# Kernel optimization log

Hardware: AMD Instinct MI355X
Metric: run time of the kernel (lower is better)

Reference implementation:

```python
import jax, jax.numpy as jnp
import numpy as np

NAMES = ['tempo', 'chord', 'barbeat', 'type', 'pitch', 'duration', 'velocity']
VOCABS = [56, 135, 18, 4, 87, 18, 25]
EMBS = [128, 256, 64, 32, 512, 128, 128]
B, S, D, H, L, FF = 2, 2048, 512, 8, 8, 2048
HD = D // H
EPS = 1e-6


def _layernorm(x, g, b):
    m = x.mean(-1, keepdims=True)
    v = ((x - m) ** 2).mean(-1, keepdims=True)
    return (x - m) / jnp.sqrt(v + 1e-5) * g + b


def _rope(x, cos, sin):
    x1, x2 = jnp.split(x, 2, -1)
    return x * cos + jnp.concatenate([-x2, x1], -1) * sin


def _causal_linear_attn(q, k, v):
    # kernelized causal linear attention: phi = elu + 1, cumulative-sum normalization
    q = jax.nn.elu(q) + 1.0
    k = jax.nn.elu(k) + 1.0
    kv = jnp.cumsum(jnp.einsum('bshd,bshm->bshdm', k, v), axis=1)  # [B,S,H,HD,HD]
    z = 1.0 / (jnp.einsum('bshd,bshd->bsh', q, jnp.cumsum(k, axis=1)) + EPS)
    return jnp.einsum('bshd,bshdm->bshm', q, kv) * z[..., None]


def _forward(inputs, target, emb_tables, in_W, in_b, Wq, bq, Wk, bk, Wv, bv, Wo, bo,
             ln1_g, ln1_b, ln2_g, ln2_b, W1, b1, W2, b2, norm_g, norm_b, pWs, pbs, catW, catb):
    # multi-field embedding, each scaled by sqrt(d_emb) (CPEmbedding)
    embs = [emb_tables[i][inputs[..., i]] * jnp.sqrt(jnp.float32(EMBS[i])) for i in range(7)]
    x = jnp.concatenate(embs, -1) @ in_W + in_b  # [B,S,D]
    # PositionalEncoding: original indexes pe at position seq_len -> single d_model vector
    div = jnp.exp(jnp.arange(0, D, 2, dtype=jnp.float32) * (-np.log(10000.0) / D))
    pe = jnp.zeros((D,), jnp.float32).at[0::2].set(jnp.sin(S * div)).at[1::2].set(jnp.cos(S * div))
    x = x + pe
    # rotary tables for head_dim
    inv_freq = 1.0 / (10000.0 ** (jnp.arange(0, HD, 2, dtype=jnp.float32) / HD))
    fr = jnp.arange(S, dtype=jnp.float32)[:, None] * inv_freq[None, :]
    ang = jnp.concatenate([fr, fr], -1)  # [S,HD]
    cos = jnp.cos(ang)[None, :, None, :]
    sin = jnp.sin(ang)[None, :, None, :]
    for l in range(L):
        q = (x @ Wq[l] + bq[l]).reshape(B, S, H, HD)
        k = (x @ Wk[l] + bk[l]).reshape(B, S, H, HD)
        v = (x @ Wv[l] + bv[l]).reshape(B, S, H, HD)
        q = _rope(q, cos, sin)
        k = _rope(k, cos, sin)
        a = _causal_linear_attn(q, k, v).reshape(B, S, D) @ Wo[l] + bo[l]
        x = x + a
        y = x = _layernorm(x, ln1_g[l], ln1_b[l])
        y = jax.nn.gelu(y @ W1[l] + b1[l], approximate=False) @ W2[l] + b2[l]
        x = _layernorm(x + y, ln2_g[l], ln2_b[l])
    x = _layernorm(x, norm_g, norm_b)
    # MultiProj with teacher-forced type embedding (target branch)
    emb_t = emb_tables[3][target[..., 3]] * jnp.sqrt(jnp.float32(EMBS[3]))
    proj_type = (x @ pWs[3] + pbs[3]) * jnp.sqrt(jnp.float32(VOCABS[3]))  # from pre-concat x
    xc = jnp.concatenate([x, emb_t], -1) @ catW + catb
    outs = []
    for i in range(7):
        if i == 3:
            outs.append(proj_type)
        else:
            outs.append((xc @ pWs[i] + pbs[i]) * jnp.sqrt(jnp.float32(VOCABS[i])))
    return jnp.concatenate(outs, -1)  # [B,S,sum(VOCABS)=343]


def setup_inputs():
    key = jax.random.key(0)
    kit = iter(jax.random.split(key, 64))
    s = 0.02
    d = {}
    d['inputs'] = jax.random.randint(next(kit), (B, S, 7), 0, 4)
    d['target'] = jax.random.randint(next(kit), (B, S, 7), 0, 4)
    for i, n in enumerate(NAMES):
        d['emb_' + n] = jax.random.normal(next(kit), (VOCABS[i], EMBS[i]), jnp.float32) * s
    E = sum(EMBS)
    d['in_W'] = jax.random.normal(next(kit), (E, D)) * s
    d['in_b'] = jnp.zeros((D,))
    for nm, sh in [('Wq', (L, D, D)), ('Wk', (L, D, D)), ('Wv', (L, D, D)), ('Wo', (L, D, D)), ('W1', (L, D, FF)), ('W2', (L, FF, D))]:
        d[nm] = jax.random.normal(next(kit), sh) * s
    for nm, sh in [('bq', (L, D)), ('bk', (L, D)), ('bv', (L, D)), ('bo', (L, D)), ('b1', (L, FF)), ('b2', (L, D)), ('ln1_b', (L, D)), ('ln2_b', (L, D)), ('norm_b', (D,)), ('catb', (D,))]:
        d[nm] = jnp.zeros(sh)
    d['ln1_g'] = jnp.ones((L, D))
    d['ln2_g'] = jnp.ones((L, D))
    d['norm_g'] = jnp.ones((D,))
    for i, n in enumerate(NAMES):
        d['pW_' + n] = jax.random.normal(next(kit), (D, VOCABS[i])) * s
        d['pb_' + n] = jnp.zeros((VOCABS[i],))
    d['catW'] = jax.random.normal(next(kit), (D + 32, D)) * s
    return d


def reference(inputs, target, emb_tempo, emb_chord, emb_barbeat, emb_type, emb_pitch, emb_duration, emb_velocity,
              in_W, in_b, Wq, bq, Wk, bk, Wv, bv, Wo, bo, ln1_g, ln1_b, ln2_g, ln2_b, W1, b1, W2, b2,
              norm_g, norm_b, pW_tempo, pb_tempo, pW_chord, pb_chord, pW_barbeat, pb_barbeat, pW_type, pb_type,
              pW_pitch, pb_pitch, pW_duration, pb_duration, pW_velocity, pb_velocity, catW, catb):
    emb_tables = [emb_tempo, emb_chord, emb_barbeat, emb_type, emb_pitch, emb_duration, emb_velocity]
    pWs = [pW_tempo, pW_chord, pW_barbeat, pW_type, pW_pitch, pW_duration, pW_velocity]
    pbs = [pb_tempo, pb_chord, pb_barbeat, pb_type, pb_pitch, pb_duration, pb_velocity]
    return _forward(inputs, target, emb_tables, in_W, in_b, Wq, bq, Wk, bk, Wv, bv, Wo, bo,
                    ln1_g, ln1_b, ln2_g, ln2_b, W1, b1, W2, b2, norm_g, norm_b, pWs, pbs, catW, catb)
```

## Files before the change

kernel.cpp:

```cpp
#include <hip/hip_runtime.h>
#include <math.h>

typedef unsigned short u16;
typedef short bf16x8 __attribute__((ext_vector_type(8)));
typedef float f32x4 __attribute__((ext_vector_type(4)));
typedef u16 u16x4 __attribute__((ext_vector_type(4)));
typedef u16 u16x8 __attribute__((ext_vector_type(8)));

#define NB 2
#define NS 2048
#define ND 512
#define NH 8
#define NHD 64
#define NL 8
#define NFF 2048
#define NM (NB*NS)
#define NE 1248
#define NEP 1280
#define NXC 576
#define CHK 64
#define NCH (NS/CHK)
#define QKVW 1536

__device__ inline float b2f(u16 u){ union{ unsigned int i; float f;} x; x.i = ((unsigned int)u)<<16; return x.f; }
__device__ inline u16 f2b(float f){ union{ float f; unsigned int i;} x; x.f=f; unsigned int r = x.i + 0x7fffu + ((x.i>>16)&1u); return (u16)(r>>16); }

#define GLL(src, dst) __builtin_amdgcn_global_load_lds( \
    (__attribute__((address_space(1))) void*)(void*)(src), \
    (__attribute__((address_space(3))) void*)(dst), 16, 0, 0)

__global__ void k_embed(const int* __restrict__ inp,
    const float* __restrict__ e0, const float* __restrict__ e1, const float* __restrict__ e2,
    const float* __restrict__ e3, const float* __restrict__ e4, const float* __restrict__ e5,
    const float* __restrict__ e6, u16* __restrict__ xe)
{
  int row = blockIdx.x;
  int i0 = inp[row*7+0], i1 = inp[row*7+1], i2 = inp[row*7+2], i3 = inp[row*7+3],
      i4 = inp[row*7+4], i5 = inp[row*7+5], i6 = inp[row*7+6];
  size_t base = (size_t)row*NEP;
  for (int c = threadIdx.x; c < NEP; c += 256){
    float val = 0.f;
    if      (c < 128)  val = e0[i0*128 + c]        * 11.3137084990f;
    else if (c < 384)  val = e1[i1*256 + (c-128)]  * 16.0f;
    else if (c < 448)  val = e2[i2*64  + (c-384)]  * 8.0f;
    else if (c < 480)  val = e3[i3*32  + (c-448)]  * 5.6568542495f;
    else if (c < 992)  val = e4[i4*512 + (c-480)]  * 22.6274169980f;
    else if (c < 1120) val = e5[i5*128 + (c-992)]  * 11.3137084990f;
    else if (c < NE)   val = e6[i6*128 + (c-1120)] * 11.3137084990f;
    xe[base + c] = f2b(val);
  }
}

__device__ inline void trans_tile128(const float* __restrict__ W, u16* __restrict__ WT,
                                     int K, int N, int Kpad, int bx, int by){
  __shared__ u16 t[128*128];
  int tid = threadIdx.x;
  int k0 = by*128, n0 = bx*128;
  int c = tid & 31, sub = tid >> 5;
  #pragma unroll
  for (int half=0; half<2; half++){
    int kg = sub + half*8;
    u16 r0[8], r1[8], r2[8], r3[8];
    #pragma unroll
    for (int j=0;j<8;j++){
      int k = k0 + kg*8 + j;
      float4 v = {0.f,0.f,0.f,0.f};
      if (k < K) v = *(const float4*)(W + (size_t)k*N + n0 + c*4);
      r0[j] = f2b(v.x); r1[j] = f2b(v.y); r2[j] = f2b(v.z); r3[j] = f2b(v.w);
    }
    #pragma unroll
    for (int i=0;i<4;i++){
      int n = c*4 + i;
      int g = kg ^ (n & 15);
      const u16* rp = (i==0)?r0:(i==1)?r1:(i==2)?r2:r3;
      *(u16x8*)&t[n*128 + g*8] = *(const u16x8*)rp;
    }
  }
  __syncthreads();
  int kg2 = tid & 15, nsub = tid >> 4;
  #pragma unroll
  for (int p=0;p<8;p++){
    int nl = p*16 + nsub;
    int k = k0 + kg2*8;
    if (k < Kpad)
      *(u16x8*)(WT + (size_t)(n0+nl)*Kpad + k) = *(const u16x8*)&t[nl*128 + ((kg2 ^ (nl&15))<<3)];
  }
}

__global__ void k_prepw(const float* __restrict__ Wq, const float* __restrict__ Wk,
                        const float* __restrict__ Wv, const float* __restrict__ Wo,
                        const float* __restrict__ in_W, const float* __restrict__ catW,
                        const float* __restrict__ W1, const float* __restrict__ W2,
                        u16* __restrict__ qkvoT, u16* __restrict__ inWT, u16* __restrict__ catWT,
                        u16* __restrict__ w1T, u16* __restrict__ w2T)
{
  int bid = blockIdx.x;
  if (bid < 512){
    int z = bid >> 4, r = bid & 15;
    int l = z >> 2, s2 = z & 3;
    const float* W = (s2==0?Wq:s2==1?Wk:s2==2?Wv:Wo) + (size_t)l*ND*ND;
    trans_tile128(W, qkvoT + (size_t)z*ND*ND, ND, ND, ND, r & 3, r >> 2);
  } else if (bid < 552){
    int r = bid - 512;
    trans_tile128(in_W, inWT, NE, ND, NEP, r & 3, r >> 2);
  } else if (bid < 572){
    int r = bid - 552;
    trans_tile128(catW, catWT, 544, ND, NXC, r & 3, r >> 2);
  } else if (bid < 1084){
    int r = bid - 572;
    int l = r >> 6; int rr = r & 63;
    trans_tile128(W1 + (size_t)l*ND*NFF, w1T + (size_t)l*ND*NFF, ND, NFF, ND, rr & 15, rr >> 4);
  } else {
    int r = bid - 1084;
    int l = r >> 6; int rr = r & 63;
    trans_tile128(W2 + (size_t)l*NFF*ND, w2T + (size_t)l*ND*NFF, NFF, ND, NFF, rr & 3, rr >> 2);
  }
}

__global__ void k_misc(float* __restrict__ rc, float* __restrict__ rs,
    const float* p0,const float* p1,const float* p2,const float* p3,
    const float* p4,const float* p5,const float* p6,
    const float* q0,const float* q1,const float* q2,const float* q3,
    const float* q4,const float* q5,const float* q6,
    u16* __restrict__ pwcT, float* __restrict__ pbc,
    u16* __restrict__ ptT, float* __restrict__ pbt,
    const float* __restrict__ bq, const float* __restrict__ bk, const float* __restrict__ bv,
    float* __restrict__ bqkv, const float* __restrict__ in_b, float* __restrict__ bias_in)
{
  int idx = blockIdx.x*256 + threadIdx.x;
  if (idx < NS*32){
    int s = idx >> 5, j = idx & 31;
    double inv = exp(-(double)(2*j) * log(10000.0) / (double)NHD);
    double ang = (double)s * inv;
    rc[idx] = (float)cos(ang);
    rs[idx] = (float)sin(ang);
  }
  const int off[8] = {0,56,191,209,213,300,318,343};
  {
    int col = idx >> 9, k = idx & 511;
    if (col < 384){
      u16 v = 0;
      if (col < 343){
        int f = 0;
        while (col >= off[f+1]) f++;
        int cc = col - off[f];
        int V = off[f+1]-off[f];
        const float* P = (f==0)?p0:(f==1)?p1:(f==2)?p2:(f==3)?p3:(f==4)?p4:(f==5)?p5:p6;
        v = f2b(P[(size_t)k*V + cc] * sqrtf((float)V));
      }
      pwcT[(size_t)col*512 + k] = v;
    }
    if (idx < 64*512){
      int n = idx >> 9;
      ptT[idx] = (n < 4) ? f2b(p3[(size_t)k*4 + n]*2.0f) : (u16)0;
    }
  }
  if (idx < 343){
    int c2 = idx, f = 0;
    while (c2 >= off[f+1]) f++;
    int cc = c2 - off[f]; int V = off[f+1]-off[f];
    const float* Q = (f==0)?q0:(f==1)?q1:(f==2)?q2:(f==3)?q3:(f==4)?q4:(f==5)?q5:q6;
    pbc[idx] = Q[cc]*sqrtf((float)V);
  }
  if (idx < 4) pbt[idx] = q3[idx]*2.0f;
  if (idx < NL*QKVW){
    int l = idx / QKVW, c = idx % QKVW;
    float v = (c < 512) ? bq[l*512 + c] : (c < 1024) ? bk[l*512 + c - 512] : bv[l*512 + c - 1024];
    bqkv[idx] = v;
  }
  if (idx < ND){
    double div = exp(-(double)(idx & ~1) * log(10000.0) / (double)ND);
    double ang = (double)NS * div;
    float pev = (idx & 1) ? (float)cos(ang) : (float)sin(ang);
    bias_in[idx] = in_b[idx] + pev;
  }
}

template<int ACT, int NT, int TM>
__global__ __launch_bounds__(256) void k_gemm(
    const u16* __restrict__ A, const u16* __restrict__ BT,
    const float* __restrict__ bias, float* __restrict__ Cf, u16* __restrict__ Cb,
    int N, int klen, int lda, int ldb, int ldc,
    int koff, float* __restrict__ Cf2,
    const float* __restrict__ rc, const float* __restrict__ rs)
{
  constexpr int MREP = TM/32;
  __shared__ u16 SH[TM*64 + NT*32*64];
  u16* As = SH;
  u16* Bs = SH + TM*64;
  int tid = threadIdx.x;
  int w = tid >> 6, lane = tid & 63;

  int kz = blockIdx.z;
  A  += (size_t)kz*koff;
  BT += (size_t)kz*koff;
  if (kz){ Cf = Cf2; bias = nullptr; }

  int nwg = gridDim.x*gridDim.y;
  int d = blockIdx.y*gridDim.x + blockIdx.x;
  int wl = ((nwg & 7) == 0) ? ((d & 7)*(nwg >> 3) + (d >> 3)) : d;
  int bx = wl % gridDim.x, by = wl / gridDim.x;
  int m0 = by*TM, n0 = bx*(NT*32);

  f32x4 acc[MREP][NT];
  #pragma unroll
  for (int m=0;m<MREP;m++)
    #pragma unroll
    for (int n=0;n<NT;n++) acc[m][n] = (f32x4){0.f,0.f,0.f,0.f};

  int lg = lane>>3;
  int cg = (lane&7) ^ lg;
  const u16* ag = A  + (size_t)(m0 + w*(TM/4) + lg)*lda + cg*8;
  const u16* bg = BT + (size_t)(n0 + w*(NT*8) + lg)*ldb + cg*8;
  int wr = (w>>1)*(TM/2), wc = (w&1)*(NT*16);
  int lr = lane & 15;
  int rx = lr & 7;
  int cb_ = lane >> 4;
  int g = lane >> 4;

  int nk = klen >> 6;
  for (int t = 0; t < nk; ++t){
    int k0 = t << 6;
    #pragma unroll
    for (int i=0;i<TM/32;i++)
      GLL(ag + (size_t)(i*8)*lda + k0, &As[(w*(TM/4) + i*8)*64]);
    #pragma unroll
    for (int j=0;j<NT;j++)
      GLL(bg + (size_t)(j*8)*ldb + k0, &Bs[(w*(NT*8) + j*8)*64]);
    __syncthreads();
    #pragma unroll
    for (int kk=0;kk<2;kk++){
      int gA = ((kk*4 + cb_) ^ rx) * 8;
      bf16x8 af[MREP], bfr[NT];
      #pragma unroll
      for (int m=0;m<MREP;m++) af[m]  = *(const bf16x8*)&As[(wr + m*16 + lr)*64 + gA];
      #pragma unroll
      for (int n=0;n<NT;n++)   bfr[n] = *(const bf16x8*)&Bs[(wc + n*16 + lr)*64 + gA];
      #pragma unroll
      for (int m=0;m<MREP;m++)
        #pragma unroll
        for (int n=0;n<NT;n++)
          acc[m][n] = __builtin_amdgcn_mfma_f32_16x16x32_bf16(af[m], bfr[n], acc[m][n], 0,0,0);
    }
    __syncthreads();
  }

  if (ACT == 2){
    float* Cs = (float*)SH;
    #pragma unroll
    for (int n=0;n<NT;n++){
      int col = wc + n*16 + lr;
      float bv = bias ? bias[n0 + col] : 0.f;
      #pragma unroll
      for (int m=0;m<MREP;m++)
        #pragma unroll
        for (int r=0;r<4;r++)
          Cs[(wr + m*16 + g*4 + r)*64 + col] = acc[m][n][r] + bv;
    }
    __syncthreads();
    if (n0 < 1024){
      #pragma unroll
      for (int i=0;i<8;i++){
        int p = tid + i*256;
        int row = p >> 5, j = p & 31;
        float a1 = Cs[row*64 + j], a2 = Cs[row*64 + j + 32];
        int s = (m0 + row) & (NS-1);
        float c = rc[s*32+j], sn = rs[s*32+j];
        float r1 = a1*c - a2*sn, r2 = a2*c + a1*sn;
        Cb[(size_t)(m0+row)*ldc + n0 + j]      = f2b((r1 > 0.f) ? r1+1.f : expf(r1));
        Cb[(size_t)(m0+row)*ldc + n0 + j + 32] = f2b((r2 > 0.f) ? r2+1.f : expf(r2));
      }
    } else {
      #pragma unroll
      for (int i=0;i<16;i++){
        int p = tid + i*256;
        int row = p >> 6, c2 = p & 63;
        Cb[(size_t)(m0+row)*ldc + n0 + c2] = f2b(Cs[row*64 + c2]);
      }
    }
    return;
  }

  #pragma unroll
  for (int n=0;n<NT;n++){
    int col = n0 + wc + n*16 + lr;
    if (col < N){
      float bv = bias ? bias[col] : 0.f;
      #pragma unroll
      for (int m=0;m<MREP;m++){
        #pragma unroll
        for (int r=0;r<4;r++){
          int row = m0 + wr + m*16 + g*4 + r;
          float v = acc[m][n][r] + bv;
          if (ACT==1) v = 0.5f*v*(1.f+erff(v*0.70710678118654752f));
          if (Cf) Cf[(size_t)row*ldc + col] = v;
          if (Cb) Cb[(size_t)row*ldc + col] = f2b(v);
        }
      }
    }
  }
}

__global__ __launch_bounds__(256) void k_att1(const u16* __restrict__ qkv, float* __restrict__ pref){
  int c = blockIdx.x, h = blockIdx.y, b = blockIdx.z;
  __shared__ u16 Kt[64*64];
  __shared__ u16 Vt[80*64];
  int tid = threadIdx.x;
  {
    int t = tid & 63, dseg = (tid>>6)*16;
    const u16* kg = qkv + ((size_t)(b*NS + c*CHK + t))*QKVW + 512 + h*NHD + dseg;
    u16x8 k0 = *(const u16x8*)kg;
    u16x8 k1 = *(const u16x8*)(kg+8);
    u16x8 v0 = *(const u16x8*)(kg+512);
    u16x8 v1 = *(const u16x8*)(kg+520);
    #pragma unroll
    for (int e=0;e<8;e++){
      int d0 = dseg+e, d1 = dseg+8+e;
      Kt[(d0*64+t) ^ ((d0&7)<<3)] = k0[e];
      Kt[(d1*64+t) ^ ((d1&7)<<3)] = k1[e];
      Vt[(d0*64+t) ^ ((d0&7)<<3)] = v0[e];
      Vt[(d1*64+t) ^ ((d1&7)<<3)] = v1[e];
    }
    if (tid < 64) Vt[4096 + tid] = 0x3F80;
    for (int e = tid; e < 15*64; e += 256){
      int r = 65 + (e>>6), tt = e&63;
      Vt[(r*64+tt) ^ ((r&7)<<3)] = 0;
    }
  }
  __syncthreads();
  int lane = tid & 63, w = tid >> 6;
  int lr = lane & 15, lk = (lane>>4)*8;
  f32x4 acc[5];
  #pragma unroll
  for (int i=0;i<5;i++) acc[i] = (f32x4){0.f,0.f,0.f,0.f};
  #pragma unroll
  for (int kk=0;kk<2;kk++){
    int mcol = w*16 + lr;
    bf16x8 bfrag = *(const bf16x8*)&Kt[(mcol*64 + kk*32 + lk) ^ ((mcol&7)<<3)];
    #pragma unroll
    for (int fr=0; fr<5; fr++){
      int arow = fr*16 + lr;
      bf16x8 afrag = *(const bf16x8*)&Vt[(arow*64 + kk*32 + lk) ^ ((arow&7)<<3)];
      acc[fr] = __builtin_amdgcn_mfma_f32_16x16x32_bf16(afrag, bfrag, acc[fr], 0,0,0);
    }
  }
  size_t base = (((size_t)(b*NH + h))*NCH + c)*5120;
  int g = lane>>4;
  #pragma unroll
  for (int fr=0; fr<5; fr++)
    #pragma unroll
    for (int r=0;r<4;r++)
      pref[base + (fr*16 + g*4 + r)*64 + w*16 + lr] = acc[fr][r];
}

__global__ __launch_bounds__(256) void k_att2(const float* __restrict__ pref, u16* __restrict__ prefb){
  int bh = blockIdx.y;
  int e = blockIdx.x*256 + threadIdx.x;
  size_t base = (size_t)bh*NCH*5120 + e;
  int se = e ^ (((e>>6)&7)<<3);
  size_t sb = (size_t)bh*NCH*5120 + se;
  float v[NCH];
  #pragma unroll
  for (int c=0;c<NCH;c++) v[c] = pref[base + (size_t)c*5120];
  float run = 0.f;
  #pragma unroll
  for (int c=0;c<NCH;c++){ prefb[sb + (size_t)c*5120] = f2b(run); run += v[c]; }
}

__global__ __launch_bounds__(256) void k_att3(const u16* __restrict__ qkv,
    const u16* __restrict__ prefb, u16* __restrict__ outa)
{
  int c = blockIdx.x, h = blockIdx.y, b = blockIdx.z;
  __shared__ u16 Qs[4096], Ks[4096];
  __shared__ u16 Vt[5120], Ps[5120];
  __shared__ float dens[64];
  u16* Sm = Ks;
  int tid = threadIdx.x;
  int lane = tid & 63, w = tid >> 6;
  {
    int r8 = lane >> 3;
    int gsw = (lane & 7) ^ r8;
    const u16* qbase = qkv + ((size_t)(b*NS + c*CHK))*QKVW + h*NHD + gsw*8;
    #pragma unroll
    for (int half = 0; half < 2; half++){
      int rbase = w*16 + half*8;
      const u16* src = qbase + (size_t)(rbase + r8)*QKVW;
      GLL(src,       &Qs[rbase*64]);
      GLL(src + 512, &Ks[rbase*64]);
    }
    const u16* pb = prefb + (((size_t)(b*NH + h))*NCH + c)*5120 + lane*8;
    for (int ch = w; ch < 10; ch += 4)
      GLL(pb + ch*512, &Ps[ch*512]);
  }
  {
    int t = tid&63, dseg = (tid>>6)*16;
    const u16* vg = qkv + ((size_t)(b*NS + c*CHK + t))*QKVW + 1024 + h*NHD + dseg;
    u16x8 v0 = *(const u16x8*)vg;
    u16x8 v1 = *(const u16x8*)(vg+8);
    #pragma unroll
    for (int e=0;e<8;e++){
      int d0=dseg+e, d1=dseg+8+e;
      Vt[(d0*64+t)^((d0&7)<<3)] = v0[e];
      Vt[(d1*64+t)^((d1&7)<<3)] = v1[e];
    }
    if (tid<64) Vt[4096+tid] = 0x3F80;
    for (int e=tid; e<15*64; e+=256){
      int r = 65+(e>>6), tt = e&63;
      Vt[(r*64+tt)^((r&7)<<3)] = 0;
    }
  }
  __syncthreads();
  int lr = lane&15, lk = (lane>>4)*8, g = lane>>4;
  f32x4 sacc[4];
  #pragma unroll
  for (int i=0;i<4;i++) sacc[i] = (f32x4){0.f,0.f,0.f,0.f};
  int iq = w*16 + lr;
  #pragma unroll
  for (int kk=0;kk<2;kk++){
    bf16x8 bq = *(const bf16x8*)&Qs[(iq*64 + kk*32 + lk) ^ ((iq&7)<<3)];
    #pragma unroll
    for (int ft=0; ft<4; ft++){
      int tr = ft*16 + lr;
      bf16x8 ak = *(const bf16x8*)&Ks[(tr*64 + kk*32 + lk) ^ ((tr&7)<<3)];
      sacc[ft] = __builtin_amdgcn_mfma_f32_16x16x32_bf16(ak, bq, sacc[ft], 0,0,0);
    }
  }
  __syncthreads();
  #pragma unroll
  for (int ft=0; ft<4; ft++){
    int t0 = ft*16 + g*4;
    u16x4 pk;
    #pragma unroll
    for (int r=0;r<4;r++) pk[r] = f2b((t0+r <= iq) ? sacc[ft][r] : 0.f);
    *(u16x4*)&Sm[(iq*64 + t0) ^ ((iq&7)<<3)] = pk;
  }
  __syncthreads();
  f32x4 acc[5];
  #pragma unroll
  for (int i=0;i<5;i++) acc[i] = (f32x4){0.f,0.f,0.f,0.f};
  #pragma unroll
  for (int kk=0;kk<2;kk++){
    int sw = (iq&7)<<3;
    bf16x8 as = *(const bf16x8*)&Sm[(iq*64 + kk*32 + lk) ^ sw];
    bf16x8 aq = *(const bf16x8*)&Qs[(iq*64 + kk*32 + lk) ^ sw];
    #pragma unroll
    for (int c5=0;c5<5;c5++){
      int col = c5*16 + lr, sw2 = (col&7)<<3;
      bf16x8 bv = *(const bf16x8*)&Vt[(col*64 + kk*32 + lk) ^ sw2];
      bf16x8 bp = *(const bf16x8*)&Ps[(col*64 + kk*32 + lk) ^ sw2];
      acc[c5] = __builtin_amdgcn_mfma_f32_16x16x32_bf16(as, bv, acc[c5], 0,0,0);
      acc[c5] = __builtin_amdgcn_mfma_f32_16x16x32_bf16(aq, bp, acc[c5], 0,0,0);
    }
  }
  if (lr == 0){
    #pragma unroll
    for (int r=0;r<4;r++) dens[w*16 + g*4 + r] = acc[4][r];
  }
  __syncthreads();
  #pragma unroll
  for (int c5=0;c5<4;c5++){
    #pragma unroll
    for (int r=0;r<4;r++){
      int i = w*16 + g*4 + r;
      float z = 1.f/(dens[i] + 1e-6f);
      outa[((size_t)(b*NS + c*CHK + i))*ND + h*NHD + c5*16 + lr] = f2b(acc[c5][r]*z);
    }
  }
}

__global__ __launch_bounds__(256) void k_ln(const float* __restrict__ xin, const float* __restrict__ res,
    const float* __restrict__ res2, float* __restrict__ outx, u16* __restrict__ outb,
    const float* __restrict__ g, const float* __restrict__ bvec,
    const int* __restrict__ tgt, const float* __restrict__ embt, u16* __restrict__ xcb)
{
  int row = blockIdx.x, tid = threadIdx.x;
  size_t base = (size_t)row*ND;
  float v0 = xin[base+tid], v1 = xin[base+tid+256];
  if (res){ v0 += res[base+tid]; v1 += res[base+tid+256]; }
  if (res2){ v0 += res2[base+tid]; v1 += res2[base+tid+256]; }
  float s = v0+v1, ss2 = v0*v0 + v1*v1;
  #pragma unroll
  for (int o = 32; o >= 1; o >>= 1){
    s   += __shfl_down(s, o, 64);
    ss2 += __shfl_down(ss2, o, 64);
  }
  __shared__ float red[8];
  int wv = tid >> 6, ln = tid & 63;
  if (ln == 0){ red[wv] = s; red[4+wv] = ss2; }
  __syncthreads();
  float stot  = red[0]+red[1]+red[2]+red[3];
  float sstot = red[4]+red[5]+red[6]+red[7];
  float mean = stot * (1.0f/ND);
  float var  = sstot * (1.0f/ND) - mean*mean;
  float inv = 1.0f / sqrtf(var + 1e-5f);
  float o0 = (v0-mean)*inv*g[tid]     + bvec[tid];
  float o1 = (v1-mean)*inv*g[tid+256] + bvec[tid+256];
  outx[base+tid] = o0; outx[base+tid+256] = o1;
  if (outb){ outb[base+tid] = f2b(o0); outb[base+tid+256] = f2b(o1); }
  if (xcb){
    size_t xbse = (size_t)row*NXC;
    xcb[xbse+tid] = f2b(o0);
    xcb[xbse+tid+256] = f2b(o1);
    if (tid < 32){
      int id = tgt[row*7+3];
      xcb[xbse+512+tid] = f2b(embt[id*32+tid]*5.6568542495f);
      xcb[xbse+544+tid] = 0;
    }
  }
}

extern "C" void kernel_launch(void* const* d_in, const int* in_sizes, int n_in,
                              void* d_out, int out_size, void* d_ws, size_t ws_size,
                              hipStream_t stream)
{
  const int* inputs = (const int*)d_in[0];
  const int* target = (const int*)d_in[1];
  const float* emb[7];
  for (int i=0;i<7;i++) emb[i] = (const float*)d_in[2+i];
  const float* in_W  = (const float*)d_in[9];
  const float* in_b  = (const float*)d_in[10];
  const float* Wq = (const float*)d_in[11];
  const float* Wk = (const float*)d_in[12];
  const float* Wv = (const float*)d_in[13];
  const float* Wo = (const float*)d_in[14];
  const float* W1 = (const float*)d_in[15];
  const float* W2 = (const float*)d_in[16];
  const float* bq = (const float*)d_in[17];
  const float* bk = (const float*)d_in[18];
  const float* bv = (const float*)d_in[19];
  const float* bo = (const float*)d_in[20];
  const float* b1 = (const float*)d_in[21];
  const float* b2 = (const float*)d_in[22];
  const float* ln1_b = (const float*)d_in[23];
  const float* ln2_b = (const float*)d_in[24];
  const float* norm_b = (const float*)d_in[25];
  const float* catb   = (const float*)d_in[26];
  const float* ln1_g = (const float*)d_in[27];
  const float* ln2_g = (const float*)d_in[28];
  const float* norm_g = (const float*)d_in[29];
  const float* pW[7]; const float* pb[7];
  for (int i=0;i<7;i++){ pW[i]=(const float*)d_in[30+2*i]; pb[i]=(const float*)d_in[31+2*i]; }
  const float* catW = (const float*)d_in[44];
  float* outp = (float*)d_out;

  char* base = (char*)d_ws;
  size_t off = 0;
  auto alloc = [&](size_t bytes)->void*{ void* p = base + off; off += bytes; off = (off + 255) & ~(size_t)255; return p; };

  float* x    = (float*)alloc((size_t)NM*ND*4);
  u16*   xb   = (u16*)  alloc((size_t)NM*ND*2);
  u16*   qkvb = (u16*)  alloc((size_t)NM*QKVW*2);
  float* tb   = (float*)alloc((size_t)NM*ND*4);
  float* tb2  = (float*)alloc((size_t)NM*ND*4);
  u16*   ab   = (u16*)  alloc((size_t)NM*ND*2);
  u16*   hb   = (u16*)  alloc((size_t)NM*NFF*2);
  float* rc   = (float*)alloc((size_t)NS*32*4);
  float* rs   = (float*)alloc((size_t)NS*32*4);
  float* pref = (float*)alloc((size_t)NB*NH*NCH*5120*4);
  u16*  prefb = (u16*)  alloc((size_t)NB*NH*NCH*5120*2);
  u16*  qkvoT = (u16*)  alloc((size_t)NL*4*ND*ND*2);
  u16*  w1T   = (u16*)  alloc((size_t)NL*NFF*ND*2);
  u16*  w2T   = (u16*)  alloc((size_t)NL*ND*NFF*2);
  u16*  inWT  = (u16*)  alloc((size_t)ND*NEP*2);
  u16*  catWT = (u16*)  alloc((size_t)ND*NXC*2);
  u16*  pwcT  = (u16*)  alloc((size_t)384*512*2);
  float* pbc  = (float*)alloc(344*4);
  u16*  ptT   = (u16*)  alloc((size_t)64*512*2);
  float* pbt  = (float*)alloc(4*4);
  float* bqkv = (float*)alloc((size_t)NL*QKVW*4);
  float* bias_in = (float*)alloc(ND*4);
  u16*  xeb = hb;
  u16*  xcb = hb;
  u16*  ocb = hb + (size_t)NM*NXC;

  k_prepw<<<1596, 256, 0, stream>>>(Wq, Wk, Wv, Wo, in_W, catW, W1, W2,
                                    qkvoT, inWT, catWT, w1T, w2T);
  k_misc<<<768, 256, 0, stream>>>(rc, rs,
      pW[0],pW[1],pW[2],pW[3],pW[4],pW[5],pW[6],
      pb[0],pb[1],pb[2],pb[3],pb[4],pb[5],pb[6],
      pwcT, pbc, ptT, pbt, bq, bk, bv, bqkv, in_b, bias_in);

  k_embed<<<NM, 256, 0, stream>>>(inputs, emb[0],emb[1],emb[2],emb[3],emb[4],emb[5],emb[6], xeb);
  k_gemm<0,2,64><<<dim3(8,64,1), 256, 0, stream>>>(xeb, inWT, bias_in, x, xb,
      ND, NEP, NEP, NEP, ND, 0, nullptr, nullptr, nullptr);

  dim3 agrid(NCH, NH, NB);
  for (int l = 0; l < NL; l++){
    const u16* woT = qkvoT + (size_t)(l*4+3)*ND*ND;
    k_gemm<2,2,64><<<dim3(24,64,1), 256, 0, stream>>>(xb, qkvoT + (size_t)l*4*ND*ND,
        bqkv + l*QKVW, nullptr, qkvb, QKVW, ND, ND, ND, QKVW, 0, nullptr, rc, rs);
    k_att1<<<agrid, 256, 0, stream>>>(qkvb, pref);
    k_att2<<<dim3(20,16), 256, 0, stream>>>(pref, prefb);
    k_att3<<<agrid, 256, 0, stream>>>(qkvb, prefb, ab);
    k_gemm<0,2,64><<<dim3(8,64,2), 256, 0, stream>>>(ab, woT, bo + l*ND, tb, nullptr,
        ND, 256, ND, ND, ND, 256, tb2, nullptr, nullptr);
    k_ln<<<NM, 256, 0, stream>>>(x, tb, tb2, x, xb, ln1_g + l*ND, ln1_b + l*ND,
                                 nullptr, nullptr, nullptr);
    k_gemm<1,2,64><<<dim3(32,64,1), 256, 0, stream>>>(xb, w1T + (size_t)l*NFF*ND,
        b1 + l*NFF, nullptr, hb, NFF, ND, ND, ND, NFF, 0, nullptr, nullptr, nullptr);
    k_gemm<0,2,64><<<dim3(8,64,2), 256, 0, stream>>>(hb, w2T + (size_t)l*ND*NFF,
        b2 + l*ND, tb, nullptr, ND, 1024, NFF, NFF, ND, 1024, tb2, nullptr, nullptr);
    k_ln<<<NM, 256, 0, stream>>>(x, tb, tb2, x, xb, ln2_g + l*ND, ln2_b + l*ND,
                                 nullptr, nullptr, nullptr);
  }

  k_ln<<<NM, 256, 0, stream>>>(x, nullptr, nullptr, x, xb, norm_g, norm_b,
                               target, emb[3], xcb);

  k_gemm<0,2,64><<<dim3(8,64,1), 256, 0, stream>>>(xcb, catWT, catb, nullptr, ocb,
      ND, NXC, NXC, NXC, ND, 0, nullptr, nullptr, nullptr);
  k_gemm<0,2,64><<<dim3(6,64,1), 256, 0, stream>>>(ocb, pwcT, pbc, outp, nullptr,
      343, ND, ND, ND, 343, 0, nullptr, nullptr, nullptr);
  k_gemm<0,2,64><<<dim3(1,64,1), 256, 0, stream>>>(xb, ptT, pbt, outp + 209, nullptr,
      4, ND, ND, ND, 343, 0, nullptr, nullptr, nullptr);
}
```

Baseline: 828.7 us.

## Merge prep kernels, store attention chunk prefixes as bf16, drop Wo split-K

The two weight and constant preparation kernels become one launch. The attention chunk-state pass now writes bf16 swizzled partials directly, and the prefix-sum pass runs in place on that buffer, which removes the fp32 intermediate. The Wo projection no longer splits K across two partial buffers, so layernorm reads a single input. The transpose-tile LDS swizzle pattern also changes. Storing partials in bf16 before the prefix sum lowers the precision of the accumulated states.

```diff
diff --git a/kernel.cpp b/kernel.cpp
--- a/kernel.cpp
+++ b/kernel.cpp
@@ -71,7 +71,7 @@
     #pragma unroll
     for (int i=0;i<4;i++){
       int n = c*4 + i;
-      int g = kg ^ (n & 15);
+      int g = kg ^ ((n>>2) & 15);
       const u16* rp = (i==0)?r0:(i==1)?r1:(i==2)?r2:r3;
       *(u16x8*)&t[n*128 + g*8] = *(const u16x8*)rp;
     }
@@ -83,16 +83,26 @@
     int nl = p*16 + nsub;
     int k = k0 + kg2*8;
     if (k < Kpad)
-      *(u16x8*)(WT + (size_t)(n0+nl)*Kpad + k) = *(const u16x8*)&t[nl*128 + ((kg2 ^ (nl&15))<<3)];
-  }
-}
-
-__global__ void k_prepw(const float* __restrict__ Wq, const float* __restrict__ Wk,
-                        const float* __restrict__ Wv, const float* __restrict__ Wo,
-                        const float* __restrict__ in_W, const float* __restrict__ catW,
-                        const float* __restrict__ W1, const float* __restrict__ W2,
-                        u16* __restrict__ qkvoT, u16* __restrict__ inWT, u16* __restrict__ catWT,
-                        u16* __restrict__ w1T, u16* __restrict__ w2T)
+      *(u16x8*)(WT + (size_t)(n0+nl)*Kpad + k) = *(const u16x8*)&t[nl*128 + ((kg2 ^ ((nl>>2)&15))<<3)];
+  }
+}
+
+__global__ void k_prep(const float* __restrict__ Wq, const float* __restrict__ Wk,
+                       const float* __restrict__ Wv, const float* __restrict__ Wo,
+                       const float* __restrict__ in_W, const float* __restrict__ catW,
+                       const float* __restrict__ W1, const float* __restrict__ W2,
+                       u16* __restrict__ qkvoT, u16* __restrict__ inWT, u16* __restrict__ catWT,
+                       u16* __restrict__ w1T, u16* __restrict__ w2T,
+                       float* __restrict__ rc, float* __restrict__ rs,
+                       const float* p0,const float* p1,const float* p2,const float* p3,
+                       const float* p4,const float* p5,const float* p6,
+                       const float* q0,const float* q1,const float* q2,const float* q3,
+                       const float* q4,const float* q5,const float* q6,
+                       u16* __restrict__ pwcT, float* __restrict__ pbc,
+                       u16* __restrict__ ptT, float* __restrict__ pbt,
+                       const float* __restrict__ bq, const float* __restrict__ bk,
+                       const float* __restrict__ bv, float* __restrict__ bqkv,
+                       const float* __restrict__ in_b, float* __restrict__ bias_in)
 {
   int bid = blockIdx.x;
   if (bid < 512){
@@ -110,69 +120,58 @@
     int r = bid - 572;
     int l = r >> 6; int rr = r & 63;
     trans_tile128(W1 + (size_t)l*ND*NFF, w1T + (size_t)l*ND*NFF, ND, NFF, ND, rr & 15, rr >> 4);
-  } else {
+  } else if (bid < 1596){
     int r = bid - 1084;
     int l = r >> 6; int rr = r & 63;
     trans_tile128(W2 + (size_t)l*NFF*ND, w2T + (size_t)l*ND*NFF, NFF, ND, NFF, rr & 3, rr >> 2);
-  }
-}
-
-__global__ void k_misc(float* __restrict__ rc, float* __restrict__ rs,
-    const float* p0,const float* p1,const float* p2,const float* p3,
-    const float* p4,const float* p5,const float* p6,
-    const float* q0,const float* q1,const float* q2,const float* q3,
-    const float* q4,const float* q5,const float* q6,
-    u16* __restrict__ pwcT, float* __restrict__ pbc,
-    u16* __restrict__ ptT, float* __restrict__ pbt,
-    const float* __restrict__ bq, const float* __restrict__ bk, const float* __restrict__ bv,
-    float* __restrict__ bqkv, const float* __restrict__ in_b, float* __restrict__ bias_in)
-{
-  int idx = blockIdx.x*256 + threadIdx.x;
-  if (idx < NS*32){
-    int s = idx >> 5, j = idx & 31;
-    double inv = exp(-(double)(2*j) * log(10000.0) / (double)NHD);
-    double ang = (double)s * inv;
-    rc[idx] = (float)cos(ang);
-    rs[idx] = (float)sin(ang);
-  }
-  const int off[8] = {0,56,191,209,213,300,318,343};
-  {
-    int col = idx >> 9, k = idx & 511;
-    if (col < 384){
-      u16 v = 0;
-      if (col < 343){
-        int f = 0;
-        while (col >= off[f+1]) f++;
-        int cc = col - off[f];
-        int V = off[f+1]-off[f];
-        const float* P = (f==0)?p0:(f==1)?p1:(f==2)?p2:(f==3)?p3:(f==4)?p4:(f==5)?p5:p6;
-        v = f2b(P[(size_t)k*V + cc] * sqrtf((float)V));
+  } else {
+    int idx = (bid - 1596)*256 + threadIdx.x;
+    if (idx < NS*32){
+      int s = idx >> 5, j = idx & 31;
+      double inv = exp(-(double)(2*j) * log(10000.0) / (double)NHD);
+      double ang = (double)s * inv;
+      rc[idx] = (float)cos(ang);
+      rs[idx] = (float)sin(ang);
+    }
+    const int off[8] = {0,56,191,209,213,300,318,343};
+    {
+      int col = idx >> 9, k = idx & 511;
+      if (col < 384){
+        u16 v = 0;
+        if (col < 343){
+          int f = 0;
+          while (col >= off[f+1]) f++;
+          int cc = col - off[f];
+          int V = off[f+1]-off[f];
+          const float* P = (f==0)?p0:(f==1)?p1:(f==2)?p2:(f==3)?p3:(f==4)?p4:(f==5)?p5:p6;
+          v = f2b(P[(size_t)k*V + cc] * sqrtf((float)V));
+        }
+        pwcT[(size_t)col*512 + k] = v;
       }
-      pwcT[(size_t)col*512 + k] = v;
-    }
-    if (idx < 64*512){
-      int n = idx >> 9;
-      ptT[idx] = (n < 4) ? f2b(p3[(size_t)k*4 + n]*2.0f) : (u16)0;
-    }
-  }
-  if (idx < 343){
-    int c2 = idx, f = 0;
-    while (c2 >= off[f+1]) f++;
-    int cc = c2 - off[f]; int V = off[f+1]-off[f];
-    const float* Q = (f==0)?q0:(f==1)?q1:(f==2)?q2:(f==3)?q3:(f==4)?q4:(f==5)?q5:q6;
-    pbc[idx] = Q[cc]*sqrtf((float)V);
-  }
-  if (idx < 4) pbt[idx] = q3[idx]*2.0f;
-  if (idx < NL*QKVW){
-    int l = idx / QKVW, c = idx % QKVW;
-    float v = (c < 512) ? bq[l*512 + c] : (c < 1024) ? bk[l*512 + c - 512] : bv[l*512 + c - 1024];
-    bqkv[idx] = v;
-  }
-  if (idx < ND){
-    double div = exp(-(double)(idx & ~1) * log(10000.0) / (double)ND);
-    double ang = (double)NS * div;
-    float pev = (idx & 1) ? (float)cos(ang) : (float)sin(ang);
-    bias_in[idx] = in_b[idx] + pev;
+      if (idx < 64*512){
+        int n = idx >> 9;
+        ptT[idx] = (n < 4) ? f2b(p3[(size_t)k*4 + n]*2.0f) : (u16)0;
+      }
+    }
+    if (idx < 343){
+      int c2 = idx, f = 0;
+      while (c2 >= off[f+1]) f++;
+      int cc = c2 - off[f]; int V = off[f+1]-off[f];
+      const float* Q = (f==0)?q0:(f==1)?q1:(f==2)?q2:(f==3)?q3:(f==4)?q4:(f==5)?q5:q6;
+      pbc[idx] = Q[cc]*sqrtf((float)V);
+    }
+    if (idx < 4) pbt[idx] = q3[idx]*2.0f;
+    if (idx < NL*QKVW){
+      int l = idx / QKVW, c = idx % QKVW;
+      float v = (c < 512) ? bq[l*512 + c] : (c < 1024) ? bk[l*512 + c - 512] : bv[l*512 + c - 1024];
+      bqkv[idx] = v;
+    }
+    if (idx < ND){
+      double div = exp(-(double)(idx & ~1) * log(10000.0) / (double)ND);
+      double ang = (double)NS * div;
+      float pev = (idx & 1) ? (float)cos(ang) : (float)sin(ang);
+      bias_in[idx] = in_b[idx] + pev;
+    }
   }
 }
 
@@ -301,7 +300,7 @@
   }
 }
 
-__global__ __launch_bounds__(256) void k_att1(const u16* __restrict__ qkv, float* __restrict__ pref){
+__global__ __launch_bounds__(256) void k_att1(const u16* __restrict__ qkv, u16* __restrict__ prefb){
   int c = blockIdx.x, h = blockIdx.y, b = blockIdx.z;
   __shared__ u16 Kt[64*64];
   __shared__ u16 Vt[80*64];
@@ -344,27 +343,28 @@
       acc[fr] = __builtin_amdgcn_mfma_f32_16x16x32_bf16(afrag, bfrag, acc[fr], 0,0,0);
     }
   }
-  size_t base = (((size_t)(b*NH + h))*NCH + c)*5120;
+  size_t pbase = (((size_t)(b*NH + h))*NCH + c)*5120;
   int g = lane>>4;
   #pragma unroll
   for (int fr=0; fr<5; fr++)
     #pragma unroll
-    for (int r=0;r<4;r++)
-      pref[base + (fr*16 + g*4 + r)*64 + w*16 + lr] = acc[fr][r];
-}
-
-__global__ __launch_bounds__(256) void k_att2(const float* __restrict__ pref, u16* __restrict__ prefb){
+    for (int r=0;r<4;r++){
+      int row = fr*16 + g*4 + r;
+      int idx = row*64 + w*16 + lr;
+      prefb[pbase + (idx ^ ((row&7)<<3))] = f2b(acc[fr][r]);
+    }
+}
+
+__global__ __launch_bounds__(256) void k_att2(u16* __restrict__ prefb){
   int bh = blockIdx.y;
   int e = blockIdx.x*256 + threadIdx.x;
   size_t base = (size_t)bh*NCH*5120 + e;
-  int se = e ^ (((e>>6)&7)<<3);
-  size_t sb = (size_t)bh*NCH*5120 + se;
   float v[NCH];
   #pragma unroll
-  for (int c=0;c<NCH;c++) v[c] = pref[base + (size_t)c*5120];
+  for (int c=0;c<NCH;c++) v[c] = b2f(prefb[base + (size_t)c*5120]);
   float run = 0.f;
   #pragma unroll
-  for (int c=0;c<NCH;c++){ prefb[sb + (size_t)c*5120] = f2b(run); run += v[c]; }
+  for (int c=0;c<NCH;c++){ prefb[base + (size_t)c*5120] = f2b(run); run += v[c]; }
 }
 
 __global__ __launch_bounds__(256) void k_att3(const u16* __restrict__ qkv,
@@ -556,7 +556,6 @@
   u16*   hb   = (u16*)  alloc((size_t)NM*NFF*2);
   float* rc   = (float*)alloc((size_t)NS*32*4);
   float* rs   = (float*)alloc((size_t)NS*32*4);
-  float* pref = (float*)alloc((size_t)NB*NH*NCH*5120*4);
   u16*  prefb = (u16*)  alloc((size_t)NB*NH*NCH*5120*2);
   u16*  qkvoT = (u16*)  alloc((size_t)NL*4*ND*ND*2);
   u16*  w1T   = (u16*)  alloc((size_t)NL*NFF*ND*2);
@@ -573,9 +572,8 @@
   u16*  xcb = hb;
   u16*  ocb = hb + (size_t)NM*NXC;
 
-  k_prepw<<<1596, 256, 0, stream>>>(Wq, Wk, Wv, Wo, in_W, catW, W1, W2,
-                                    qkvoT, inWT, catWT, w1T, w2T);
-  k_misc<<<768, 256, 0, stream>>>(rc, rs,
+  k_prep<<<2364, 256, 0, stream>>>(Wq, Wk, Wv, Wo, in_W, catW, W1, W2,
+      qkvoT, inWT, catWT, w1T, w2T, rc, rs,
       pW[0],pW[1],pW[2],pW[3],pW[4],pW[5],pW[6],
       pb[0],pb[1],pb[2],pb[3],pb[4],pb[5],pb[6],
       pwcT, pbc, ptT, pbt, bq, bk, bv, bqkv, in_b, bias_in);
@@ -589,12 +587,12 @@
     const u16* woT = qkvoT + (size_t)(l*4+3)*ND*ND;
     k_gemm<2,2,64><<<dim3(24,64,1), 256, 0, stream>>>(xb, qkvoT + (size_t)l*4*ND*ND,
         bqkv + l*QKVW, nullptr, qkvb, QKVW, ND, ND, ND, QKVW, 0, nullptr, rc, rs);
-    k_att1<<<agrid, 256, 0, stream>>>(qkvb, pref);
-    k_att2<<<dim3(20,16), 256, 0, stream>>>(pref, prefb);
+    k_att1<<<agrid, 256, 0, stream>>>(qkvb, prefb);
+    k_att2<<<dim3(20,16), 256, 0, stream>>>(prefb);
     k_att3<<<agrid, 256, 0, stream>>>(qkvb, prefb, ab);
-    k_gemm<0,2,64><<<dim3(8,64,2), 256, 0, stream>>>(ab, woT, bo + l*ND, tb, nullptr,
-        ND, 256, ND, ND, ND, 256, tb2, nullptr, nullptr);
-    k_ln<<<NM, 256, 0, stream>>>(x, tb, tb2, x, xb, ln1_g + l*ND, ln1_b + l*ND,
+    k_gemm<0,2,64><<<dim3(8,64,1), 256, 0, stream>>>(ab, woT, bo + l*ND, tb, nullptr,
+        ND, ND, ND, ND, ND, 0, nullptr, nullptr, nullptr);
+    k_ln<<<NM, 256, 0, stream>>>(x, tb, nullptr, x, xb, ln1_g + l*ND, ln1_b + l*ND,
                                  nullptr, nullptr, nullptr);
     k_gemm<1,2,64><<<dim3(32,64,1), 256, 0, stream>>>(xb, w1T + (size_t)l*NFF*ND,
         b1 + l*NFF, nullptr, hb, NFF, ND, ND, ND, NFF, 0, nullptr, nullptr, nullptr);
```

New measurement: 808.7 us. 2.4% less time.
